# Optimization experiments

Hardware: AMD Instinct MI355X
Metric: run time of the kernel (lower is better)

## Reference

```python
import jax, jax.numpy as jnp
import numpy as np
import math

B, S, H, D = 4, 4096, 16, 64

def setup_inputs() -> dict:
    key = jax.random.key(0)
    k1, k2 = jax.random.split(key)
    qkv = jax.random.normal(k1, (B, S, 3, H, D), dtype=jnp.float32)
    key_padding_mask = jax.random.randint(k2, (B, S), 0, 2).astype(jnp.bool_)
    return {"qkv": qkv, "key_padding_mask": key_padding_mask}

def reference(qkv, key_padding_mask):
    # Faithful to FlashAtten_pytorch2_func: qkv (nnz,3,h,d) is unsqueezed to
    # (1,nnz,h,d) before SDPA, so SDPA treats nnz as batch and the HEADS dim
    # as the sequence dim -> each token attends over its own heads (h x h).
    # The unpad/pad round-trip is therefore equivalent to per-token attention
    # followed by zeroing padded positions (index_put into zeros buffer).
    q = qkv[:, :, 0]  # (B,S,H,D)
    k = qkv[:, :, 1]
    v = qkv[:, :, 2]
    scale = 1.0 / math.sqrt(D)  # softmax_scale=None -> 1/sqrt(headdim)
    scores = jnp.einsum('bshd,bsgd->bshg', q, k) * scale  # (B,S,H,H)
    attn = jax.nn.softmax(scores, axis=-1)
    out = jnp.einsum('bshg,bsgd->bshd', attn, v)  # (B,S,H,D)
    # padded tokens were never scattered back -> remain zero
    out = out * key_padding_mask[:, :, None, None].astype(out.dtype)
    return out
```

## Files before the change

kernel.cpp:

```cpp
#include <hip/hip_runtime.h>
#include <hip/hip_bf16.h>


typedef __attribute__((ext_vector_type(8))) short short8;
typedef __attribute__((ext_vector_type(4))) float floatx4;

static __device__ __forceinline__ short f2bf(float x) {
    union { __hip_bfloat16 b; short s; } u; u.b = __float2bfloat16(x);
    return u.s;
}
static __device__ __forceinline__ float bf2f(short s) {
    union { float f; unsigned int u; } u;
    u.u = ((unsigned int)(unsigned short)s) << 16;
    return u.f;
}
static __device__ __forceinline__ void split8(floatx4 a, floatx4 b,
                                              short8& hi, short8& lo) {
    float v[8] = {a[0], a[1], a[2], a[3], b[0], b[1], b[2], b[3]};
    #pragma unroll
    for (int j = 0; j < 8; ++j) {
        short h = f2bf(v[j]);
        hi[j] = h;
        lo[j] = f2bf(v[j] - bf2f(h));
    }
}

__global__ void detect_mask_fmt(const unsigned char* __restrict__ mb, int npos,
                                int* __restrict__ flag)
{
    __shared__ int found1, found2;
    if (threadIdx.x == 0) { found1 = 0; found2 = 0; }
    __syncthreads();
    int l1 = 0;
    for (int i = threadIdx.x; i < npos; i += blockDim.x)
        if ((i & 3) != 0 && mb[i] != 0) l1 = 1;
    if (l1) atomicOr(&found1, 1);
    __syncthreads();
    if (found1 == 0) {
        int l2 = 0;
        for (int i = threadIdx.x; i < npos / 2; i += blockDim.x)
            if (mb[8 * i + 4] != 0) l2 = 1;
        if (l2) atomicOr(&found2, 1);
        __syncthreads();
    } else {
        __syncthreads();
    }
    if (threadIdx.x == 0) *flag = found1 ? 0 : (found2 ? 1 : 2);
}

__global__ __launch_bounds__(256) void fa_heads_kernel(
    const float* __restrict__ qkv,
    const unsigned char* __restrict__ maskraw,
    const int* __restrict__ fmt,
    float* __restrict__ out,
    int npos)
{
    const int wid = (blockIdx.x << 2) + (threadIdx.x >> 6);
    if (wid >= npos) return;
    const int lane = threadIdx.x & 63;
    const int t  = lane & 15;
    const int qa = lane >> 4;

    const float* base = qkv + (size_t)wid * 3072;
    const float* Qp = base;
    const float* Kp = base + 1024;
    const float* Vp = base + 2048;

    const int fo = t * 64 + qa * 8;
    short8 khi0, klo0, khi1, klo1, qhi0, qlo0, qhi1, qlo1;
    split8(*(const floatx4*)(Kp + fo),      *(const floatx4*)(Kp + fo + 4),  khi0, klo0);
    split8(*(const floatx4*)(Kp + fo + 32), *(const floatx4*)(Kp + fo + 36), khi1, klo1);
    split8(*(const floatx4*)(Qp + fo),      *(const floatx4*)(Qp + fo + 4),  qhi0, qlo0);
    split8(*(const floatx4*)(Qp + fo + 32), *(const floatx4*)(Qp + fo + 36), qhi1, qlo1);

    floatx4 sc = {0.f, 0.f, 0.f, 0.f};
    sc = __builtin_amdgcn_mfma_f32_16x16x32_bf16(khi0, qhi0, sc, 0, 0, 0);
    sc = __builtin_amdgcn_mfma_f32_16x16x32_bf16(khi1, qhi1, sc, 0, 0, 0);
    sc = __builtin_amdgcn_mfma_f32_16x16x32_bf16(khi0, qlo0, sc, 0, 0, 0);
    sc = __builtin_amdgcn_mfma_f32_16x16x32_bf16(khi1, qlo1, sc, 0, 0, 0);
    sc = __builtin_amdgcn_mfma_f32_16x16x32_bf16(klo0, qhi0, sc, 0, 0, 0);
    sc = __builtin_amdgcn_mfma_f32_16x16x32_bf16(klo1, qhi1, sc, 0, 0, 0);

    float s0 = sc[0] * 0.125f, s1 = sc[1] * 0.125f;
    float s2 = sc[2] * 0.125f, s3 = sc[3] * 0.125f;
    float m = fmaxf(fmaxf(s0, s1), fmaxf(s2, s3));
    m = fmaxf(m, __shfl_xor(m, 16));
    m = fmaxf(m, __shfl_xor(m, 32));
    float e0 = __expf(s0 - m), e1 = __expf(s1 - m);
    float e2 = __expf(s2 - m), e3 = __expf(s3 - m);
    float l = e0 + e1 + e2 + e3;
    l += __shfl_xor(l, 16);
    l += __shfl_xor(l, 32);
    float rl = 1.0f / l;
    float p0 = e0 * rl, p1 = e1 * rl, p2 = e2 * rl, p3 = e3 * rl;

    int slo = (t + 32 * qa) & 63;
    int shi = (slo + 16) & 63;
    float av[8];
    av[0] = __shfl(p0, slo); av[1] = __shfl(p1, slo);
    av[2] = __shfl(p2, slo); av[3] = __shfl(p3, slo);
    av[4] = __shfl(p0, shi); av[5] = __shfl(p1, shi);
    av[6] = __shfl(p2, shi); av[7] = __shfl(p3, shi);
    const bool live = (qa < 2);
    short8 aph, apl;
    #pragma unroll
    for (int j = 0; j < 8; ++j) {
        short h = live ? f2bf(av[j]) : (short)0;
        aph[j] = h;
        apl[j] = live ? f2bf(av[j] - bf2f(h)) : (short)0;
    }

    floatx4 o[4];
    #pragma unroll
    for (int c = 0; c < 4; ++c) {
        short8 bvh, bvl;
        #pragma unroll
        for (int j = 0; j < 8; ++j) {
            int g = (8 * qa + j) & 15;
            float v = Vp[g * 64 + c * 16 + t];
            short h = f2bf(v);
            bvh[j] = h;
            bvl[j] = f2bf(v - bf2f(h));
        }
        floatx4 z = {0.f, 0.f, 0.f, 0.f};
        z = __builtin_amdgcn_mfma_f32_16x16x32_bf16(aph, bvh, z, 0, 0, 0);
        z = __builtin_amdgcn_mfma_f32_16x16x32_bf16(aph, bvl, z, 0, 0, 0);
        z = __builtin_amdgcn_mfma_f32_16x16x32_bf16(apl, bvh, z, 0, 0, 0);
        o[c] = z;
    }

    const int f = *fmt;
    int mi;
    if (f == 0)       mi = (int)maskraw[wid];
    else if (f == 1)  mi = ((const int*)maskraw)[wid];
    else              mi = (int)(((const long long*)maskraw)[wid] != 0);
    const float mv = (mi != 0) ? 1.0f : 0.0f;

    float* op = out + (size_t)wid * 1024;
    #pragma unroll
    for (int c = 0; c < 4; ++c) {
        #pragma unroll
        for (int r = 0; r < 4; ++r) {
            op[(4 * qa + r) * 64 + c * 16 + t] = o[c][r] * mv;
        }
    }
}

extern "C" void kernel_launch(void* const* d_in, const int* in_sizes, int n_in,
                              void* d_out, int out_size, void* d_ws, size_t ws_size,
                              hipStream_t stream) {
    const float* qkv = (const float*)d_in[0];
    const unsigned char* maskraw = (const unsigned char*)d_in[1];
    float* out = (float*)d_out;
    int* fmt = (int*)d_ws;
    const int npos = in_sizes[1];

    detect_mask_fmt<<<1, 256, 0, stream>>>(maskraw, npos, fmt);

    const int blocks = (npos + 3) / 4;
    fa_heads_kernel<<<blocks, 256, 0, stream>>>(qkv, maskraw, fmt, out, npos);
}
```

Measured before the change: 330.8 us.

## Stage per-token QKV and output through swizzled LDS for coalesced global access

Each block now loads the QKV data for its four tokens into shared memory with wide vector loads spread across all threads. Q/K rows use an XOR swizzle, and V is stored transposed so each lane can read its operands as floatx4 vectors instead of strided scalar loads. Outputs are written back into each wave's LDS region and then stored to global memory as contiguous vector stores. The cost is 48KB of LDS per block, which limits occupancy, plus a block-wide barrier before compute.

```diff
diff --git a/kernel.cpp b/kernel.cpp
--- a/kernel.cpp
+++ b/kernel.cpp
@@ -55,23 +55,58 @@
     float* __restrict__ out,
     int npos)
 {
-    const int wid = (blockIdx.x << 2) + (threadIdx.x >> 6);
+    __shared__ float lds[4 * 3072];
+
+    const int tid  = threadIdx.x;
+    const int w    = tid >> 6;
+    const int lane = tid & 63;
+    const int posBase = blockIdx.x << 2;
+
+    {
+        const int r     = tid >> 4;
+        const int cbase = (tid & 15) << 2;
+        #pragma unroll
+        for (int p = 0; p < 4; ++p) {
+            const int pos = posBase + p;
+            if (pos >= npos) break;
+            const float* src = qkv + (size_t)pos * 3072 + tid * 4;
+            const int po = p * 3072;
+            #pragma unroll
+            for (int it = 0; it < 2; ++it) {
+                floatx4 v = *(const floatx4*)(src + it * 1024);
+                const int row = it * 16 + r;
+                const int sw  = (row & 3) << 3;
+                *(floatx4*)&lds[po + row * 64 + (cbase ^ sw)] = v;
+            }
+            {
+                floatx4 v = *(const floatx4*)(src + 2048);
+                #pragma unroll
+                for (int i = 0; i < 4; ++i) {
+                    const int d = cbase + i;
+                    lds[po + 2048 + d * 16 + (r ^ ((d & 1) << 3))] = v[i];
+                }
+            }
+        }
+    }
+    __syncthreads();
+
+    const int wid = posBase + w;
     if (wid >= npos) return;
-    const int lane = threadIdx.x & 63;
     const int t  = lane & 15;
     const int qa = lane >> 4;
+    const int po = w * 3072;
 
-    const float* base = qkv + (size_t)wid * 3072;
-    const float* Qp = base;
-    const float* Kp = base + 1024;
-    const float* Vp = base + 2048;
+    const int sw  = (t & 3) << 3;
+    const int qrow = po + t * 64;
+    const int krow = po + (16 + t) * 64;
+    const int j0  = (8 * qa) ^ sw;
+    const int j1  = ((8 * qa + 32) ^ sw);
 
-    const int fo = t * 64 + qa * 8;
     short8 khi0, klo0, khi1, klo1, qhi0, qlo0, qhi1, qlo1;
-    split8(*(const floatx4*)(Kp + fo),      *(const floatx4*)(Kp + fo + 4),  khi0, klo0);
-    split8(*(const floatx4*)(Kp + fo + 32), *(const floatx4*)(Kp + fo + 36), khi1, klo1);
-    split8(*(const floatx4*)(Qp + fo),      *(const floatx4*)(Qp + fo + 4),  qhi0, qlo0);
-    split8(*(const floatx4*)(Qp + fo + 32), *(const floatx4*)(Qp + fo + 36), qhi1, qlo1);
+    split8(*(const floatx4*)&lds[krow + j0], *(const floatx4*)&lds[krow + j0 + 4], khi0, klo0);
+    split8(*(const floatx4*)&lds[krow + j1], *(const floatx4*)&lds[krow + j1 + 4], khi1, klo1);
+    split8(*(const floatx4*)&lds[qrow + j0], *(const floatx4*)&lds[qrow + j0 + 4], qhi0, qlo0);
+    split8(*(const floatx4*)&lds[qrow + j1], *(const floatx4*)&lds[qrow + j1 + 4], qhi1, qlo1);
 
     floatx4 sc = {0.f, 0.f, 0.f, 0.f};
     sc = __builtin_amdgcn_mfma_f32_16x16x32_bf16(khi0, qhi0, sc, 0, 0, 0);
@@ -113,15 +148,12 @@
     floatx4 o[4];
     #pragma unroll
     for (int c = 0; c < 4; ++c) {
+        const int d = 16 * c + t;
+        const int vb = po + 2048 + d * 16 + ((8 * (qa & 1)) ^ ((d & 1) << 3));
+        floatx4 v0 = *(const floatx4*)&lds[vb];
+        floatx4 v1 = *(const floatx4*)&lds[vb + 4];
         short8 bvh, bvl;
-        #pragma unroll
-        for (int j = 0; j < 8; ++j) {
-            int g = (8 * qa + j) & 15;
-            float v = Vp[g * 64 + c * 16 + t];
-            short h = f2bf(v);
-            bvh[j] = h;
-            bvl[j] = f2bf(v - bf2f(h));
-        }
+        split8(v0, v1, bvh, bvl);
         floatx4 z = {0.f, 0.f, 0.f, 0.f};
         z = __builtin_amdgcn_mfma_f32_16x16x32_bf16(aph, bvh, z, 0, 0, 0);
         z = __builtin_amdgcn_mfma_f32_16x16x32_bf16(aph, bvl, z, 0, 0, 0);
@@ -136,13 +168,18 @@
     else              mi = (int)(((const long long*)maskraw)[wid] != 0);
     const float mv = (mi != 0) ? 1.0f : 0.0f;
 
-    float* op = out + (size_t)wid * 1024;
     #pragma unroll
     for (int c = 0; c < 4; ++c) {
         #pragma unroll
         for (int r = 0; r < 4; ++r) {
-            op[(4 * qa + r) * 64 + c * 16 + t] = o[c][r] * mv;
+            lds[po + (4 * qa + r) * 64 + c * 16 + t] = o[c][r] * mv;
         }
+    }
+    float* op = out + (size_t)wid * 1024;
+    #pragma unroll
+    for (int k = 0; k < 4; ++k) {
+        floatx4 v = *(const floatx4*)&lds[po + k * 256 + lane * 4];
+        *(floatx4*)(op + k * 256 + lane * 4) = v;
     }
 }
 
```

Result: no change. 332.4 us (+0.5%).
